# Kernel optimization log

Hardware: AMD Instinct MI355X
Metric: run time of the kernel (lower is better)

Reference implementation:

```python
import jax, jax.numpy as jnp
import numpy as np

B, N, S, K, R = 4, 8192, 2048, 64, 0.2  # batch, points, centroids, neighbors, ball radius
EPS = 1e-5  # BatchNorm eps


def fps_indices(x, n_samples):
    """Farthest point sampling; returns int32 [B, n_samples] indices."""
    xs = jax.lax.stop_gradient(x)
    Bb, Nn, _ = xs.shape

    def step(carry, _):
        dist, farthest = carry
        centroid = jnp.take_along_axis(xs, farthest[:, None, None], axis=1)  # [B,1,3]
        d = jnp.sum((xs - centroid) ** 2, axis=-1)  # [B,N]
        dist = jnp.minimum(dist, d)
        nxt = jnp.argmax(dist, axis=-1).astype(jnp.int32)
        return (dist, nxt), farthest

    init = (jnp.full((Bb, Nn), 1e10, xs.dtype), jnp.zeros((Bb,), jnp.int32))
    _, idxs = jax.lax.scan(step, init, None, length=n_samples)  # [S,B]
    return jnp.transpose(idxs)  # [B,S]


def ball_query(x, centroids, radius, k):
    """First k point indices within radius of each centroid, -1 padded. int32 [B,S,k]."""
    xs = jax.lax.stop_gradient(x)
    cs = jax.lax.stop_gradient(centroids)
    Nn = xs.shape[1]
    d2 = jnp.sum((cs[:, :, None, :] - xs[:, None, :, :]) ** 2, axis=-1)  # [B,S,N]
    cand = jnp.where(d2 < radius * radius, jnp.arange(Nn, dtype=jnp.int32), Nn)
    neg_topk, _ = jax.lax.top_k(-cand, k)  # k smallest candidate indices
    idx = -neg_topk
    return jnp.where(idx == Nn, -1, idx)


def _forward(x, x_complete, layers, idx_fps, idx_ball):
    centroids = jnp.take_along_axis(x, idx_fps[..., None], axis=1)  # [B,S,3]
    valid = idx_ball >= 0  # [B,S,K]
    sidx = jnp.maximum(idx_ball, 0)
    gather = lambda pts: jax.vmap(lambda p, i: p[i])(pts, sidx)  # [B,S,K,C]
    x_local = gather(x) - centroids[:, :, None, :]  # relative coords
    feats = jnp.concatenate([gather(x_complete), x_local], axis=-1)  # [B,S,K,67]
    h = feats.reshape(B, S * K, -1).transpose(0, 2, 1)  # [B,67,S*K]
    for (W, b, g, bt, m, v) in layers:  # Conv1d(k=1) -> BN(eval) -> ReLU
        h = jnp.einsum('oc,bcn->bon', W, h) + b[None, :, None]
        h = (h - m[None, :, None]) * (g * jax.lax.rsqrt(v + EPS))[None, :, None] + bt[None, :, None]
        h = jax.nn.relu(h)
    h = h.reshape(B, -1, S, K)  # [B,128,S,K]
    h = jnp.where(valid[:, None, :, :], h, -jnp.inf)  # mask invalid neighbors
    pooled = jnp.max(h, axis=3)  # masked max pool over neighborhood
    return centroids, pooled.transpose(0, 2, 1)  # [B,S,3], [B,S,128]


def setup_inputs():
    key = jax.random.key(0)
    ks = jax.random.split(key, 8)
    x = jax.random.uniform(ks[0], (B, N, 3), jnp.float32)
    x_complete = jax.random.normal(ks[1], (B, N, 64), jnp.float32)
    dims = [67, 64, 64, 128]
    inp = {'x': x, 'x_complete': x_complete}
    for i in range(3):
        cin, cout = dims[i], dims[i + 1]
        kk = jax.random.split(ks[2 + i], 6)
        inp[f'W{i+1}'] = jax.random.normal(kk[0], (cout, cin), jnp.float32) * 0.05
        inp[f'b{i+1}'] = jax.random.normal(kk[1], (cout,), jnp.float32) * 0.02
        inp[f'g{i+1}'] = 1.0 + 0.1 * jax.random.normal(kk[2], (cout,), jnp.float32)
        inp[f'bt{i+1}'] = jax.random.normal(kk[3], (cout,), jnp.float32) * 0.02
        inp[f'm{i+1}'] = jax.random.normal(kk[4], (cout,), jnp.float32) * 0.05
        inp[f'v{i+1}'] = jax.random.uniform(kk[5], (cout,), jnp.float32, minval=0.5, maxval=1.5)
    return inp


def reference(x, x_complete, W1, b1, g1, bt1, m1, v1, W2, b2, g2, bt2, m2, v2, W3, b3, g3, bt3, m3, v3):
    idx_fps = fps_indices(x, S)
    cen_sg = jnp.take_along_axis(jax.lax.stop_gradient(x), idx_fps[..., None], axis=1)
    idx_ball = ball_query(x, cen_sg, R, K)
    layers = ((W1, b1, g1, bt1, m1, v1), (W2, b2, g2, bt2, m2, v2), (W3, b3, g3, bt3, m3, v3))
    return _forward(x, x_complete, layers, idx_fps, idx_ball)
```

## Files before the change

kernel.cpp:

```cpp
#include <hip/hip_runtime.h>
#include <math.h>

#define BATCH 4
#define NPTS  8192
#define NSAMP 2048
#define KNBR  64
#define EPSF  1e-5f

__global__ void prep_kernel(const float* __restrict__ W1, const float* __restrict__ W2,
                            const float* __restrict__ W3,
                            float* __restrict__ W1t, float* __restrict__ W2t,
                            float* __restrict__ W3t) {
    int t = threadIdx.x;
    for (int i = t; i < 64 * 67; i += 256) { int o = i / 67, c = i % 67; W1t[c * 64 + o] = W1[i]; }
    for (int i = t; i < 64 * 64; i += 256) { int o = i >> 6, c = i & 63; W2t[c * 64 + o] = W2[i]; }
    for (int i = t; i < 128 * 64; i += 256) { int o = i >> 6, c = i & 63; W3t[c * 128 + o] = W3[i]; }
}

#define DPP_FMAX(v, ctrl)                                                            \
    do {                                                                             \
        int _t = __builtin_amdgcn_update_dpp(0, __float_as_int(v), ctrl, 0xf, 0xf, true); \
        (v) = fmaxf((v), __int_as_float(_t));                                        \
    } while (0)

__global__ __launch_bounds__(512) void fps_kernel(const float* __restrict__ x,
                                                  float* __restrict__ cen_out) {
    const int b = blockIdx.x;
    const int tid = threadIdx.x;
    const int lane = tid & 63;
    const int wid = tid >> 6;
    __shared__ float sx[NPTS], sy[NPTS], sz[NPTS];
    __shared__ __align__(16) float pd[2][8];
    __shared__ __align__(16) int pi[2][8];
    __shared__ int hist[NSAMP];

    const float* xb = x + (size_t)b * NPTS * 3;
    for (int i = tid; i < NPTS; i += 512) {
        sx[i] = xb[3 * i + 0];
        sy[i] = xb[3 * i + 1];
        sz[i] = xb[3 * i + 2];
    }
    __syncthreads();

    float px[16], py[16], pz[16], dist[16];
#pragma unroll
    for (int j = 0; j < 16; j++) {
        int p = tid * 16 + j;
        px[j] = sx[p]; py[j] = sy[p]; pz[j] = sz[p];
        dist[j] = 1e10f;
    }

    int cur = 0;
    for (int s = 0; s < NSAMP; s++) {
        float cx = sx[cur], cy = sy[cur], cz = sz[cur];
        if (tid == 0) hist[s] = cur;
        float bestd = -1.0f;
        int bestj = 0;
#pragma unroll
        for (int j = 0; j < 16; j++) {
            float dx = __fsub_rn(px[j], cx);
            float dy = __fsub_rn(py[j], cy);
            float dz = __fsub_rn(pz[j], cz);
            float d = __fadd_rn(__fadd_rn(__fmul_rn(dx, dx), __fmul_rn(dy, dy)), __fmul_rn(dz, dz));
            float dm = fminf(dist[j], d);
            dist[j] = dm;
            if (dm > bestd) { bestd = dm; bestj = j; }
        }
        float w = bestd;
        DPP_FMAX(w, 0x111);
        DPP_FMAX(w, 0x112);
        DPP_FMAX(w, 0x114);
        DPP_FMAX(w, 0x118);
        DPP_FMAX(w, 0x142);
        DPP_FMAX(w, 0x143);
        float wmax = __int_as_float(__builtin_amdgcn_readlane(__float_as_int(w), 63));
        unsigned long long eq = __ballot(bestd == wmax);
        int src = __ffsll(eq) - 1;
        int widx = __builtin_amdgcn_readlane(tid * 16 + bestj, src);
        const int p = s & 1;
        if (lane == 0) { pd[p][wid] = wmax; pi[p][wid] = widx; }
        __syncthreads();
        float4 da = *(const float4*)&pd[p][0];
        float4 db = *(const float4*)&pd[p][4];
        int4 ia = *(const int4*)&pi[p][0];
        int4 ib = *(const int4*)&pi[p][4];
        float d01 = da.x; int i01 = ia.x; if (da.y > d01) { d01 = da.y; i01 = ia.y; }
        float d23 = da.z; int i23 = ia.z; if (da.w > d23) { d23 = da.w; i23 = ia.w; }
        float d45 = db.x; int i45 = ib.x; if (db.y > d45) { d45 = db.y; i45 = ib.y; }
        float d67 = db.z; int i67 = ib.z; if (db.w > d67) { d67 = db.w; i67 = ib.w; }
        if (d23 > d01) { d01 = d23; i01 = i23; }
        if (d67 > d45) { d45 = d67; i45 = i67; }
        if (d45 > d01) { i01 = i45; }
        cur = i01;
    }

    __syncthreads();
    for (int i = tid; i < NSAMP; i += 512) {
        int idx = hist[i];
        float* o = cen_out + ((size_t)b * NSAMP + i) * 3;
        o[0] = sx[idx]; o[1] = sy[idx]; o[2] = sz[idx];
    }
}

__global__ __launch_bounds__(256) void ball_kernel(const float* __restrict__ x,
                                                   const float* __restrict__ cen,
                                                   int* __restrict__ idxb) {
    const int wid = threadIdx.x >> 6, lane = threadIdx.x & 63;
    const int id = blockIdx.x * 4 + wid;
    const int b = id >> 11;
    const float r2 = (float)(0.2 * 0.2);
    const float cx = cen[3 * id], cy = cen[3 * id + 1], cz = cen[3 * id + 2];
    const float* xb = x + (size_t)b * NPTS * 3;

    int count = 0;
    for (int base = 0; base < NPTS && count < KNBR; base += 64) {
        int p = base + lane;
        float pxv = xb[3 * p], pyv = xb[3 * p + 1], pzv = xb[3 * p + 2];
        float dx = __fsub_rn(cx, pxv);
        float dy = __fsub_rn(cy, pyv);
        float dz = __fsub_rn(cz, pzv);
        float d2 = __fadd_rn(__fadd_rn(__fmul_rn(dx, dx), __fmul_rn(dy, dy)), __fmul_rn(dz, dz));
        bool hit = d2 < r2;
        unsigned long long m = __ballot(hit);
        if (hit) {
            int pos = count + __popcll(m & ((1ull << lane) - 1ull));
            if (pos < KNBR) idxb[(size_t)id * KNBR + pos] = p;
        }
        count += (int)__popcll(m);
    }
    for (int pos = count + lane; pos < KNBR; pos += 64)
        idxb[(size_t)id * KNBR + pos] = -1;
}

__global__ __launch_bounds__(256) void mlp_kernel(
    const float* __restrict__ x, const float* __restrict__ xc,
    const float* __restrict__ cen, const int* __restrict__ idxb,
    const float* __restrict__ W1t, const float* __restrict__ b1, const float* __restrict__ g1,
    const float* __restrict__ bt1, const float* __restrict__ m1, const float* __restrict__ v1,
    const float* __restrict__ W2t, const float* __restrict__ b2, const float* __restrict__ g2,
    const float* __restrict__ bt2, const float* __restrict__ m2, const float* __restrict__ v2,
    const float* __restrict__ W3t, const float* __restrict__ b3, const float* __restrict__ g3,
    const float* __restrict__ bt3, const float* __restrict__ m3, const float* __restrict__ v3,
    float* __restrict__ pooled) {
    const int wid = threadIdx.x >> 6, lane = threadIdx.x & 63;
    const int id = blockIdx.x * 4 + wid;
    const int b = id >> 11;
    __shared__ float sred[4][64][33];

    int il = idxb[(size_t)id * KNBR + lane];
    bool valid = il >= 0;
    int ik = valid ? il : 0;

    float cx = cen[3 * id], cy = cen[3 * id + 1], cz = cen[3 * id + 2];
    const float* xp = x + ((size_t)b * NPTS + ik) * 3;
    const float* xcp = xc + ((size_t)b * NPTS + ik) * 64;

    float h1[64];
#pragma unroll
    for (int o = 0; o < 64; o++) h1[o] = 0.f;
#pragma unroll
    for (int c4 = 0; c4 < 16; c4++) {
        float4 t = ((const float4*)xcp)[c4];
        float tv0 = t.x, tv1 = t.y, tv2 = t.z, tv3 = t.w;
#pragma unroll
        for (int o = 0; o < 64; o++) h1[o] = fmaf(W1t[(c4 * 4 + 0) * 64 + o], tv0, h1[o]);
#pragma unroll
        for (int o = 0; o < 64; o++) h1[o] = fmaf(W1t[(c4 * 4 + 1) * 64 + o], tv1, h1[o]);
#pragma unroll
        for (int o = 0; o < 64; o++) h1[o] = fmaf(W1t[(c4 * 4 + 2) * 64 + o], tv2, h1[o]);
#pragma unroll
        for (int o = 0; o < 64; o++) h1[o] = fmaf(W1t[(c4 * 4 + 3) * 64 + o], tv3, h1[o]);
    }
    {
        float xl0 = xp[0] - cx, xl1 = xp[1] - cy, xl2 = xp[2] - cz;
#pragma unroll
        for (int o = 0; o < 64; o++) h1[o] = fmaf(W1t[64 * 64 + o], xl0, h1[o]);
#pragma unroll
        for (int o = 0; o < 64; o++) h1[o] = fmaf(W1t[65 * 64 + o], xl1, h1[o]);
#pragma unroll
        for (int o = 0; o < 64; o++) h1[o] = fmaf(W1t[66 * 64 + o], xl2, h1[o]);
    }
#pragma unroll
    for (int o = 0; o < 64; o++) {
        float sc = g1[o] * rsqrtf(v1[o] + EPSF);
        h1[o] = fmaxf(fmaf(h1[o] + b1[o] - m1[o], sc, bt1[o]), 0.f);
    }

    float h2[64];
#pragma unroll
    for (int o = 0; o < 64; o++) h2[o] = 0.f;
#pragma unroll
    for (int c = 0; c < 64; c++) {
        float hv = h1[c];
#pragma unroll
        for (int o = 0; o < 64; o++) h2[o] = fmaf(W2t[c * 64 + o], hv, h2[o]);
    }
#pragma unroll
    for (int o = 0; o < 64; o++) {
        float sc = g2[o] * rsqrtf(v2[o] + EPSF);
        h2[o] = fmaxf(fmaf(h2[o] + b2[o] - m2[o], sc, bt2[o]), 0.f);
    }

    for (int ch = 0; ch < 4; ch++) {
        float acc[32];
#pragma unroll
        for (int oo = 0; oo < 32; oo++) acc[oo] = 0.f;
#pragma unroll
        for (int c = 0; c < 64; c++) {
            float hv = h2[c];
#pragma unroll
            for (int oo = 0; oo < 32; oo++)
                acc[oo] = fmaf(W3t[c * 128 + ch * 32 + oo], hv, acc[oo]);
        }
#pragma unroll
        for (int oo = 0; oo < 32; oo++) {
            int o = ch * 32 + oo;
            float sc = g3[o] * rsqrtf(v3[o] + EPSF);
            float t = fmaxf(fmaf(acc[oo] + b3[o] - m3[o], sc, bt3[o]), 0.f);
            sred[wid][lane][oo] = valid ? t : -INFINITY;
        }
        __syncthreads();
        {
            int c = lane & 31, half = lane >> 5;
            float mx = -INFINITY;
#pragma unroll
            for (int r = 0; r < 32; r++) mx = fmaxf(mx, sred[wid][half * 32 + r][c]);
            mx = fmaxf(mx, __shfl_xor(mx, 32, 64));
            if (lane < 32) pooled[(size_t)id * 128 + ch * 32 + c] = mx;
        }
        __syncthreads();
    }
}

extern "C" void kernel_launch(void* const* d_in, const int* in_sizes, int n_in,
                              void* d_out, int out_size, void* d_ws, size_t ws_size,
                              hipStream_t stream) {
    const float* x  = (const float*)d_in[0];
    const float* xc = (const float*)d_in[1];
    const float* W1 = (const float*)d_in[2];
    const float* b1 = (const float*)d_in[3];
    const float* g1 = (const float*)d_in[4];
    const float* bt1 = (const float*)d_in[5];
    const float* m1 = (const float*)d_in[6];
    const float* v1 = (const float*)d_in[7];
    const float* W2 = (const float*)d_in[8];
    const float* b2 = (const float*)d_in[9];
    const float* g2 = (const float*)d_in[10];
    const float* bt2 = (const float*)d_in[11];
    const float* m2 = (const float*)d_in[12];
    const float* v2 = (const float*)d_in[13];
    const float* W3 = (const float*)d_in[14];
    const float* b3 = (const float*)d_in[15];
    const float* g3 = (const float*)d_in[16];
    const float* bt3 = (const float*)d_in[17];
    const float* m3 = (const float*)d_in[18];
    const float* v3 = (const float*)d_in[19];

    float* out = (float*)d_out;
    float* cen = out;
    float* pooled = out + (size_t)BATCH * NSAMP * 3;

    int* idxb = (int*)d_ws;
    float* W1t = (float*)((char*)d_ws + (size_t)BATCH * NSAMP * KNBR * 4);
    float* W2t = W1t + 67 * 64;
    float* W3t = W2t + 64 * 64;

    prep_kernel<<<1, 256, 0, stream>>>(W1, W2, W3, W1t, W2t, W3t);
    fps_kernel<<<BATCH, 512, 0, stream>>>(x, cen);
    ball_kernel<<<(BATCH * NSAMP) / 4, 256, 0, stream>>>(x, cen, idxb);
    mlp_kernel<<<(BATCH * NSAMP) / 4, 256, 0, stream>>>(
        x, xc, cen, idxb,
        W1t, b1, g1, bt1, m1, v1,
        W2t, b2, g2, bt2, m2, v2,
        W3t, b3, g3, bt3, m3, v3,
        pooled);
}
```

Baseline: 2.429 ms.

## Pack FPS distance math into float2 and resolve argmax via atomicMin

Measured after the change: 2.419 ms. About the same (-0.4%).

```diff
diff --git a/kernel.cpp b/kernel.cpp
--- a/kernel.cpp
+++ b/kernel.cpp
@@ -6,6 +6,8 @@
 #define NSAMP 2048
 #define KNBR  64
 #define EPSF  1e-5f
+
+typedef float v2f __attribute__((ext_vector_type(2)));
 
 __global__ void prep_kernel(const float* __restrict__ W1, const float* __restrict__ W2,
                             const float* __restrict__ W3,
@@ -25,13 +27,14 @@
 
 __global__ __launch_bounds__(512) void fps_kernel(const float* __restrict__ x,
                                                   float* __restrict__ cen_out) {
+#pragma clang fp contract(off)
     const int b = blockIdx.x;
     const int tid = threadIdx.x;
     const int lane = tid & 63;
     const int wid = tid >> 6;
     __shared__ float sx[NPTS], sy[NPTS], sz[NPTS];
     __shared__ __align__(16) float pd[2][8];
-    __shared__ __align__(16) int pi[2][8];
+    __shared__ int pi[2];
     __shared__ int hist[NSAMP];
 
     const float* xb = x + (size_t)b * NPTS * 3;
@@ -40,32 +43,39 @@
         sy[i] = xb[3 * i + 1];
         sz[i] = xb[3 * i + 2];
     }
+    if (tid == 0) { pi[0] = 0x7fffffff; pi[1] = 0x7fffffff; }
     __syncthreads();
 
-    float px[16], py[16], pz[16], dist[16];
-#pragma unroll
-    for (int j = 0; j < 16; j++) {
-        int p = tid * 16 + j;
-        px[j] = sx[p]; py[j] = sy[p]; pz[j] = sz[p];
-        dist[j] = 1e10f;
+    v2f px[8], py[8], pz[8], dist[8];
+#pragma unroll
+    for (int j = 0; j < 8; j++) {
+        int p = tid * 16 + 2 * j;
+        px[j] = (v2f){sx[p], sx[p + 1]};
+        py[j] = (v2f){sy[p], sy[p + 1]};
+        pz[j] = (v2f){sz[p], sz[p + 1]};
+        dist[j] = (v2f){1e10f, 1e10f};
     }
 
     int cur = 0;
     for (int s = 0; s < NSAMP; s++) {
         float cx = sx[cur], cy = sy[cur], cz = sz[cur];
         if (tid == 0) hist[s] = cur;
-        float bestd = -1.0f;
-        int bestj = 0;
-#pragma unroll
-        for (int j = 0; j < 16; j++) {
-            float dx = __fsub_rn(px[j], cx);
-            float dy = __fsub_rn(py[j], cy);
-            float dz = __fsub_rn(pz[j], cz);
-            float d = __fadd_rn(__fadd_rn(__fmul_rn(dx, dx), __fmul_rn(dy, dy)), __fmul_rn(dz, dz));
-            float dm = fminf(dist[j], d);
+        const v2f cvx = (v2f){cx, cx}, cvy = (v2f){cy, cy}, cvz = (v2f){cz, cz};
+        v2f m = (v2f){-1.0f, -1.0f};
+#pragma unroll
+        for (int j = 0; j < 8; j++) {
+            v2f dx = px[j] - cvx;
+            v2f dy = py[j] - cvy;
+            v2f dz = pz[j] - cvz;
+            v2f d = ((dx * dx) + (dy * dy)) + (dz * dz);
+            v2f dm;
+            dm.x = fminf(dist[j].x, d.x);
+            dm.y = fminf(dist[j].y, d.y);
             dist[j] = dm;
-            if (dm > bestd) { bestd = dm; bestj = j; }
-        }
+            m.x = fmaxf(m.x, dm.x);
+            m.y = fmaxf(m.y, dm.y);
+        }
+        float bestd = fmaxf(m.x, m.y);
         float w = bestd;
         DPP_FMAX(w, 0x111);
         DPP_FMAX(w, 0x112);
@@ -73,25 +83,23 @@
         DPP_FMAX(w, 0x118);
         DPP_FMAX(w, 0x142);
         DPP_FMAX(w, 0x143);
-        float wmax = __int_as_float(__builtin_amdgcn_readlane(__float_as_int(w), 63));
-        unsigned long long eq = __ballot(bestd == wmax);
-        int src = __ffsll(eq) - 1;
-        int widx = __builtin_amdgcn_readlane(tid * 16 + bestj, src);
         const int p = s & 1;
-        if (lane == 0) { pd[p][wid] = wmax; pi[p][wid] = widx; }
+        if (lane == 63) pd[p][wid] = w;
         __syncthreads();
         float4 da = *(const float4*)&pd[p][0];
         float4 db = *(const float4*)&pd[p][4];
-        int4 ia = *(const int4*)&pi[p][0];
-        int4 ib = *(const int4*)&pi[p][4];
-        float d01 = da.x; int i01 = ia.x; if (da.y > d01) { d01 = da.y; i01 = ia.y; }
-        float d23 = da.z; int i23 = ia.z; if (da.w > d23) { d23 = da.w; i23 = ia.w; }
-        float d45 = db.x; int i45 = ib.x; if (db.y > d45) { d45 = db.y; i45 = ib.y; }
-        float d67 = db.z; int i67 = ib.z; if (db.w > d67) { d67 = db.w; i67 = ib.w; }
-        if (d23 > d01) { d01 = d23; i01 = i23; }
-        if (d67 > d45) { d45 = d67; i45 = i67; }
-        if (d45 > d01) { i01 = i45; }
-        cur = i01;
+        float bmax = fmaxf(fmaxf(fmaxf(da.x, da.y), fmaxf(da.z, da.w)),
+                           fmaxf(fmaxf(db.x, db.y), fmaxf(db.z, db.w)));
+        if (tid == 0) pi[1 - p] = 0x7fffffff;
+        int local = 0x7fffffff;
+#pragma unroll
+        for (int j = 0; j < 8; j++) {
+            if (dist[j].x == bmax) local = min(local, tid * 16 + 2 * j);
+            if (dist[j].y == bmax) local = min(local, tid * 16 + 2 * j + 1);
+        }
+        if (local != 0x7fffffff) atomicMin(&pi[p], local);
+        __syncthreads();
+        cur = pi[p];
     }
 
     __syncthreads();
```
